# Optimization experiments

Measured on AMD Instinct MI355X. Metric: run time of the kernel, lower is better.

Reference implementation:

```python
import jax, jax.numpy as jnp
import numpy as np

PRUNE_N = 2  # entries zeroed per group
PRUNE_M = 4  # group size along feature dim


def _prune_2of4(x_flat):
    # x_flat: [N, D]; zero out the PRUNE_N smallest-|.| entries in every
    # contiguous group of PRUNE_M columns (matches torch topk(largest=False)
    # + scatter mask semantics, deterministic sort-order tie-breaking).
    N, D = x_flat.shape
    g = x_flat.reshape(N, D // PRUNE_M, PRUNE_M)           # [N, G, 4]
    a = jnp.abs(g)
    order = jnp.argsort(a, axis=-1)                         # ascending |.|
    rank = jnp.argsort(order, axis=-1)                      # rank of each slot
    keep = rank >= PRUNE_N                                  # keep 2 largest
    return jnp.where(keep, g, jnp.zeros_like(g)).reshape(N, D)


def setup_inputs() -> dict:
    key = jax.random.key(0)
    k1, k2 = jax.random.split(key)
    B, S, D_IN, D_OUT = 2, 4096, 4096, 4096
    x = jax.random.normal(k1, (B, S, D_IN), dtype=jnp.float32)
    weight = jax.random.normal(k2, (D_OUT, D_IN), dtype=jnp.float32) * 0.02
    return {"x": x, "weight": weight}


def reference(x, weight):
    B, S, D = x.shape
    x_flat = x.reshape(B * S, D)
    x_sp = _prune_2of4(x_flat)                              # [B*S, D]
    out = x_sp @ weight.T                                   # [B*S, D_out]
    return out
```

## Files before the change

### kernel.cpp

```cpp
#include <hip/hip_runtime.h>
#include <hip/hip_bf16.h>

typedef float f32x4 __attribute__((ext_vector_type(4)));
typedef __bf16 bf16x8 __attribute__((ext_vector_type(8)));
typedef unsigned short ushort_t;
typedef ushort_t u16x8 __attribute__((ext_vector_type(8)));

__device__ inline ushort_t f2bf_rne(float f) {
  unsigned u = __builtin_bit_cast(unsigned, f);
  unsigned r = (u + 0x7fffu + ((u >> 16) & 1u)) >> 16;
  return (ushort_t)r;
}

__global__ void prep_kernel(const float* __restrict__ x,
                            const float* __restrict__ w,
                            ushort_t* __restrict__ xsp,
                            ushort_t* __restrict__ wb, long n8x, long n8tot) {
  long i = (long)blockIdx.x * blockDim.x + threadIdx.x;
  if (i >= n8tot) return;
  if (i < n8x) {
    const float4* p = reinterpret_cast<const float4*>(x);
    float4 g0 = p[2 * i];
    float4 g1 = p[2 * i + 1];
    float v[8] = {g0.x, g0.y, g0.z, g0.w, g1.x, g1.y, g1.z, g1.w};
    u16x8 o;
#pragma unroll
    for (int g = 0; g < 2; ++g) {
      float a[4];
#pragma unroll
      for (int j = 0; j < 4; ++j) a[j] = fabsf(v[g * 4 + j]);
#pragma unroll
      for (int j = 0; j < 4; ++j) {
        int rank = 0;
#pragma unroll
        for (int k = 0; k < 4; ++k) {
          if (k == j) continue;
          rank += (a[k] < a[j]) || (a[k] == a[j] && k < j);
        }
        o[g * 4 + j] = (rank >= 2) ? f2bf_rne(v[g * 4 + j]) : (ushort_t)0;
      }
    }
    reinterpret_cast<u16x8*>(xsp)[i] = o;
  } else {
    long j = i - n8x;
    const float4* p = reinterpret_cast<const float4*>(w);
    float4 g0 = p[2 * j];
    float4 g1 = p[2 * j + 1];
    u16x8 o;
    o[0] = f2bf_rne(g0.x); o[1] = f2bf_rne(g0.y);
    o[2] = f2bf_rne(g0.z); o[3] = f2bf_rne(g0.w);
    o[4] = f2bf_rne(g1.x); o[5] = f2bf_rne(g1.y);
    o[6] = f2bf_rne(g1.z); o[7] = f2bf_rne(g1.w);
    reinterpret_cast<u16x8*>(wb)[j] = o;
  }
}

#define BARM()                              \
  asm volatile("" ::: "memory");            \
  __builtin_amdgcn_s_barrier();             \
  asm volatile("" ::: "memory");
#define WAIT_VM4() asm volatile("s_waitcnt vmcnt(4)" ::: "memory")
#define WAIT_VM0() asm volatile("s_waitcnt vmcnt(0)" ::: "memory")

#define STAGE_A(t1, h, par)                                                    \
  {                                                                            \
    const ushort_t* g0 =                                                       \
        A + (a_row0 + (h) * 128 + srow) * (long)Kd + (t1) * 64 + scol;         \
    const ushort_t* g1 =                                                       \
        A + (a_row0 + (h) * 128 + srow + 8) * (long)Kd + (t1) * 64 + scol;     \
    ushort_t* l0 = &ldsA[((par) * 2 + (h)) * 8192 + w * 1024];                 \
    __builtin_amdgcn_global_load_lds(                                          \
        (const __attribute__((address_space(1))) void*)g0,                     \
        (__attribute__((address_space(3))) void*)l0, 16, 0, 0);                \
    __builtin_amdgcn_global_load_lds(                                          \
        (const __attribute__((address_space(1))) void*)g1,                     \
        (__attribute__((address_space(3))) void*)(l0 + 512), 16, 0, 0);        \
  }

#define STAGE_B(t1, h, par)                                                    \
  {                                                                            \
    const ushort_t* g0 =                                                       \
        B + (b_row0 + (h) * 128 + srow) * (long)Kd + (t1) * 64 + scol;         \
    const ushort_t* g1 =                                                       \
        B + (b_row0 + (h) * 128 + srow + 8) * (long)Kd + (t1) * 64 + scol;     \
    ushort_t* l0 = &ldsB[((par) * 2 + (h)) * 8192 + w * 1024];                 \
    __builtin_amdgcn_global_load_lds(                                          \
        (const __attribute__((address_space(1))) void*)g0,                     \
        (__attribute__((address_space(3))) void*)l0, 16, 0, 0);                \
    __builtin_amdgcn_global_load_lds(                                          \
        (const __attribute__((address_space(1))) void*)g1,                     \
        (__attribute__((address_space(3))) void*)(l0 + 512), 16, 0, 0);        \
  }

#define LDA_FRAG(dst, par, mi, s)                                              \
  dst = *reinterpret_cast<const bf16x8*>(                                      \
      reinterpret_cast<const char*>(ldsA) + ((par) * 2 + wr) * 16384 +         \
      (mi) * 2048 + ((s) ? roff1 : roff0));

#define LDB_FRAG(dst, par, ni, s)                                              \
  dst = *reinterpret_cast<const bf16x8*>(                                      \
      reinterpret_cast<const char*>(ldsB) + ((par) * 2 + (wc >> 1)) * 16384 +  \
      (wc & 1) * 8192 + (ni) * 2048 + ((s) ? roff1 : roff0));

#define MFMA_Q(MH, NH)                                                         \
  __builtin_amdgcn_s_setprio(1);                                               \
  _Pragma("unroll") for (int s = 0; s < 2; ++s)                                \
  _Pragma("unroll") for (int mi = 0; mi < 4; ++mi)                             \
  _Pragma("unroll") for (int ni = 0; ni < 2; ++ni)                             \
      acc[(MH) * 4 + mi][(NH) * 2 + ni] =                                      \
          __builtin_amdgcn_mfma_f32_16x16x32_bf16(                             \
              af[mi][s], bfr[(NH) * 2 + ni][s],                                \
              acc[(MH) * 4 + mi][(NH) * 2 + ni], 0, 0, 0);                     \
  __builtin_amdgcn_s_setprio(0);

#define KTILE(t, PAR)                                                          \
  {                                                                            \
    const int tA = ((t) + 1 < NT) ? (t) + 1 : NT - 1;                          \
    const int tB = ((t) + 2 < NT) ? (t) + 2 : NT - 1;                          \
            \
    _Pragma("unroll") for (int mi = 0; mi < 4; ++mi)                           \
    _Pragma("unroll") for (int s = 0; s < 2; ++s)                              \
        LDA_FRAG(af[mi][s], PAR, mi, s)                                        \
    _Pragma("unroll") for (int ni = 0; ni < 4; ++ni)                           \
    _Pragma("unroll") for (int s = 0; s < 2; ++s)                              \
        LDB_FRAG(bfr[ni][s], PAR, ni, s)                                       \
    STAGE_A(tA, 0, (PAR) ^ 1)                                                  \
    STAGE_A(tA, 1, (PAR) ^ 1)                                                  \
    MFMA_Q(0, 0)                                                               \
    MFMA_Q(0, 1)                                                               \
    _Pragma("unroll") for (int mi = 0; mi < 4; ++mi)                           \
    _Pragma("unroll") for (int s = 0; s < 2; ++s)                              \
        LDA_FRAG(af[mi][s], PAR, 4 + mi, s)                                    \
    MFMA_Q(1, 1)                                                               \
                     \
    BARM()                                                                     \
    STAGE_B(tB, 0, PAR)                                                        \
    STAGE_B(tB, 1, PAR)                                                        \
    MFMA_Q(1, 0)                                                               \
    if ((t) + 2 < NT) { WAIT_VM4(); } else { WAIT_VM0(); }                     \
    BARM()                                                                     \
  }

__global__ __launch_bounds__(512, 1) void gemm256_kernel(
    const ushort_t* __restrict__ A,
    const ushort_t* __restrict__ B,
    float* __restrict__ C,
    int M, int N, int Kd) {
  __shared__ ushort_t ldsA[4 * 8192];
  __shared__ ushort_t ldsB[4 * 8192];

  const int tid = threadIdx.x;
  const int lane = tid & 63;
  const int w = tid >> 6;
  const int wr = w >> 2;
  const int wc = w & 3;

  const int b = blockIdx.x;
  const int wg = (b & 7) * (gridDim.x >> 3) + (b >> 3);
  const int nbn = N / 256;
  const int bm = wg / nbn, bn = wg % nbn;
  const long a_row0 = (long)bm * 256;
  const long b_row0 = (long)bn * 256;
  const int NT = Kd / 64;

  const int srow = w * 16 + (lane >> 3);
  const int scol = (((lane & 7) ^ ((lane >> 3) & 7)) << 3);

  const int rl = lane & 15;
  const int q = lane >> 4;
  const int roff0 = rl * 128 + (((q) ^ (rl & 7)) << 4);
  const int roff1 = rl * 128 + (((q | 4) ^ (rl & 7)) << 4);

  f32x4 acc[8][4];
#pragma unroll
  for (int i = 0; i < 8; ++i)
#pragma unroll
    for (int j = 0; j < 4; ++j) acc[i][j] = f32x4{0.f, 0.f, 0.f, 0.f};

  bf16x8 af[4][2];
  bf16x8 bfr[4][2];

  STAGE_A(0, 0, 0)
  STAGE_A(0, 1, 0)
  STAGE_B(0, 0, 0)
  STAGE_B(0, 1, 0)
  STAGE_B(1, 0, 1)
  STAGE_B(1, 1, 1)
  WAIT_VM4();
  BARM()

  for (int t = 0; t < NT; t += 2) {
    KTILE(t, 0)
    KTILE(t + 1, 1)
  }
  WAIT_VM0();

  const int orow = (lane >> 4) * 4;
  const int ocol = lane & 15;
#pragma unroll
  for (int mi = 0; mi < 8; ++mi)
#pragma unroll
    for (int ni = 0; ni < 4; ++ni) {
      const long r0 = a_row0 + wr * 128 + mi * 16 + orow;
      const long c0 = b_row0 + wc * 64 + ni * 16 + ocol;
#pragma unroll
      for (int r = 0; r < 4; ++r) C[(r0 + r) * N + c0] = acc[mi][ni][r];
    }
}

extern "C" void kernel_launch(void* const* d_in, const int* in_sizes, int n_in,
                              void* d_out, int out_size, void* d_ws,
                              size_t ws_size, hipStream_t stream) {
  const float* x = (const float*)d_in[0];
  const float* w = (const float*)d_in[1];
  float* out = (float*)d_out;

  const int K = 4096;
  const long M = (long)in_sizes[0] / K;
  const int N = in_sizes[1] / K;

  ushort_t* xsp = (ushort_t*)d_ws;
  ushort_t* wb = xsp + (long)M * K;

  const long n8x = M * K / 8;
  const long n8w = (long)N * K / 8;
  const long n8tot = n8x + n8w;
  prep_kernel<<<(int)((n8tot + 255) / 256), 256, 0, stream>>>(x, w, xsp, wb,
                                                              n8x, n8tot);

  const int nwg = (int)(M / 256) * (N / 256);
  gemm256_kernel<<<nwg, 512, 0, stream>>>(xsp, wb, out, (int)M, N, K);
}
```

Baseline: 264.9 us.

## Restructure K-tile pipeline into four barrier-separated MFMA phases with staggered staging

Reorganizes each K-tile iteration into four phases, each loading a subset of A/B fragments from LDS, issuing one global-to-LDS stage, then running an MFMA quadrant between barriers. Global prefetch of A and B tiles is staggered across phases (B half 1 one tile ahead, A and B half 0 two tiles ahead), with prologue and vmcnt thresholds changed to match. The aim is to interleave LDS reads, global loads and MFMA work more finely, in the style of ping-pong schedules. It adds extra barriers and lgkmcnt waits, and relies on the reordered buffer reuse staying race-free.

Result: slower. 279.2 us (+5.4%).

```diff
diff --git a/kernel.cpp b/kernel.cpp
--- a/kernel.cpp
+++ b/kernel.cpp
@@ -59,7 +59,8 @@
   asm volatile("" ::: "memory");            \
   __builtin_amdgcn_s_barrier();             \
   asm volatile("" ::: "memory");
-#define WAIT_VM4() asm volatile("s_waitcnt vmcnt(4)" ::: "memory")
+#define WAIT_LGKM0() asm volatile("s_waitcnt lgkmcnt(0)" ::: "memory")
+#define WAIT_VM6() asm volatile("s_waitcnt vmcnt(6)" ::: "memory")
 #define WAIT_VM0() asm volatile("s_waitcnt vmcnt(0)" ::: "memory")
 
 #define STAGE_A(t1, h, par)                                                    \
@@ -102,42 +103,55 @@
       reinterpret_cast<const char*>(ldsB) + ((par) * 2 + (wc >> 1)) * 16384 +  \
       (wc & 1) * 8192 + (ni) * 2048 + ((s) ? roff1 : roff0));
 
-#define MFMA_Q(MH, NH)                                                         \
+#define MFMA_C(AF, BF, MH, NH)                                                 \
   __builtin_amdgcn_s_setprio(1);                                               \
   _Pragma("unroll") for (int s = 0; s < 2; ++s)                                \
   _Pragma("unroll") for (int mi = 0; mi < 4; ++mi)                             \
   _Pragma("unroll") for (int ni = 0; ni < 2; ++ni)                             \
       acc[(MH) * 4 + mi][(NH) * 2 + ni] =                                      \
           __builtin_amdgcn_mfma_f32_16x16x32_bf16(                             \
-              af[mi][s], bfr[(NH) * 2 + ni][s],                                \
-              acc[(MH) * 4 + mi][(NH) * 2 + ni], 0, 0, 0);                     \
+              AF[mi][s], BF[ni][s], acc[(MH) * 4 + mi][(NH) * 2 + ni],         \
+              0, 0, 0);                                                        \
   __builtin_amdgcn_s_setprio(0);
 
 #define KTILE(t, PAR)                                                          \
   {                                                                            \
-    const int tA = ((t) + 1 < NT) ? (t) + 1 : NT - 1;                          \
-    const int tB = ((t) + 2 < NT) ? (t) + 2 : NT - 1;                          \
-            \
+    const int tN = ((t) + 1 < NT) ? (t) + 1 : NT - 1;                          \
+    const int tC = ((t) + 2 < NT) ? (t) + 2 : NT - 1;                          \
+                     \
     _Pragma("unroll") for (int mi = 0; mi < 4; ++mi)                           \
     _Pragma("unroll") for (int s = 0; s < 2; ++s)                              \
-        LDA_FRAG(af[mi][s], PAR, mi, s)                                        \
-    _Pragma("unroll") for (int ni = 0; ni < 4; ++ni)                           \
-    _Pragma("unroll") for (int s = 0; s < 2; ++s)                              \
-        LDB_FRAG(bfr[ni][s], PAR, ni, s)                                       \
-    STAGE_A(tA, 0, (PAR) ^ 1)                                                  \
-    STAGE_A(tA, 1, (PAR) ^ 1)                                                  \
-    MFMA_Q(0, 0)                                                               \
-    MFMA_Q(0, 1)                                                               \
+        LDA_FRAG(afE[mi][s], PAR, mi, s)                                       \
+    _Pragma("unroll") for (int ni = 0; ni < 2; ++ni)                           \
+    _Pragma("unroll") for (int s = 0; s < 2; ++s)                              \
+        LDB_FRAG(b01[ni][s], PAR, ni, s)                                       \
+    STAGE_B(tN, 1, (PAR) ^ 1)                                                  \
+    BARM()                                                                     \
+    WAIT_LGKM0();                                                              \
+    MFMA_C(afE, b01, 0, 0)                                                     \
+    BARM()                                                                     \
+                             \
     _Pragma("unroll") for (int mi = 0; mi < 4; ++mi)                           \
     _Pragma("unroll") for (int s = 0; s < 2; ++s)                              \
-        LDA_FRAG(af[mi][s], PAR, 4 + mi, s)                                    \
-    MFMA_Q(1, 1)                                                               \
-                     \
-    BARM()                                                                     \
-    STAGE_B(tB, 0, PAR)                                                        \
-    STAGE_B(tB, 1, PAR)                                                        \
-    MFMA_Q(1, 0)                                                               \
-    if ((t) + 2 < NT) { WAIT_VM4(); } else { WAIT_VM0(); }                     \
+        LDA_FRAG(afO[mi][s], PAR, 4 + mi, s)                                   \
+    STAGE_A(tC, 0, PAR)                                                        \
+    BARM()                                                                     \
+    WAIT_LGKM0();                                                              \
+    MFMA_C(afO, b01, 1, 0)                                                     \
+    BARM()                                                                     \
+                             \
+    _Pragma("unroll") for (int ni = 0; ni < 2; ++ni)                           \
+    _Pragma("unroll") for (int s = 0; s < 2; ++s)                              \
+        LDB_FRAG(b23[ni][s], PAR, 2 + ni, s)                                   \
+    STAGE_A(tC, 1, PAR)                                                        \
+    BARM()                                                                     \
+    WAIT_LGKM0();                                                              \
+    MFMA_C(afO, b23, 1, 1)                                                     \
+    BARM()                                                                     \
+                   \
+    STAGE_B(tC, 0, PAR)                                                        \
+    MFMA_C(afE, b23, 0, 1)                                                     \
+    if ((t) + 2 < NT) { WAIT_VM6(); } else { WAIT_VM0(); }                     \
     BARM()                                                                     \
   }
 
@@ -177,16 +191,19 @@
 #pragma unroll
     for (int j = 0; j < 4; ++j) acc[i][j] = f32x4{0.f, 0.f, 0.f, 0.f};
 
-  bf16x8 af[4][2];
-  bf16x8 bfr[4][2];
+  bf16x8 afE[4][2];
+  bf16x8 afO[4][2];
+  bf16x8 b01[2][2];
+  bf16x8 b23[2][2];
 
   STAGE_A(0, 0, 0)
   STAGE_A(0, 1, 0)
   STAGE_B(0, 0, 0)
   STAGE_B(0, 1, 0)
+  STAGE_A(1, 0, 1)
+  STAGE_A(1, 1, 1)
   STAGE_B(1, 0, 1)
-  STAGE_B(1, 1, 1)
-  WAIT_VM4();
+  WAIT_VM6();
   BARM()
 
   for (int t = 0; t < NT; t += 2) {
```
